# Kernel optimization log

Measured on AMD Instinct MI355X. Metric: run time of the kernel, lower is better.

Reference implementation:

```python
import jax, jax.numpy as jnp
import numpy as np


def setup_inputs() -> dict:
    key = jax.random.key(0)
    k1, k2, k3 = jax.random.split(key, 3)
    B, T, J, D = 32, 1024, 128, 256  # D = 2 * input_dim
    ctx_embd = jax.random.normal(k1, (B, T, D), dtype=jnp.float32)
    query_embd = jax.random.normal(k2, (B, J, D), dtype=jnp.float32)
    # nn.Linear(6*input_dim, 1, bias=False) weight flattened: [w1 | w2 | w3], each of size D
    w = jax.random.normal(k3, (3 * D,), dtype=jnp.float32) * (1.0 / np.sqrt(3 * D))
    return {"ctx_embd": ctx_embd, "query_embd": query_embd, "w": w}


def reference(ctx_embd, query_embd, w):
    D = ctx_embd.shape[-1]
    w1, w2, w3 = w[:D], w[D:2 * D], w[2 * D:]
    # Trilinear score S[b,t,j] = ctx.w1 + query.w2 + (ctx*query).w3, decomposed
    # (algebraically identical to Linear(cat(ctx, query, ctx*query))).
    s_ctx = ctx_embd @ w1            # [B, T]
    s_qry = query_embd @ w2          # [B, J]
    s_mul = jnp.einsum('btd,bjd->btj', ctx_embd * w3, query_embd)  # [B, T, J]
    S = s_ctx[:, :, None] + s_qry[:, None, :] + s_mul              # [B, T, J]
    # Context-to-query attention
    a = jax.nn.softmax(S, axis=-1)                                 # [B, T, J]
    c2q = jnp.einsum('btj,bjd->btd', a, query_embd)                # [B, T, D]
    # Query-to-context attention
    b = jax.nn.softmax(jnp.max(S, axis=2), axis=-1)                # [B, T]
    q2c = jnp.einsum('bt,btd->bd', b, ctx_embd)[:, None, :]        # [B, 1, D] broadcast over T
    G = jnp.concatenate(
        [ctx_embd, c2q, ctx_embd * c2q, ctx_embd * q2c], axis=-1)  # [B, T, 4D]
    return G
```

## Files before the change

kernel.cpp:

```cpp
#include <hip/hip_runtime.h>

typedef float f4 __attribute__((ext_vector_type(4)));
typedef short s8v __attribute__((ext_vector_type(8)));
typedef unsigned int u4v __attribute__((ext_vector_type(4)));

#define B_ 32
#define T_ 1024
#define J_ 128
#define D_ 256

__device__ inline unsigned short f2bf(float x) {
    unsigned int u = __float_as_uint(x);
    u += 0x7fffu + ((u >> 16) & 1u);
    return (unsigned short)(u >> 16);
}
__device__ inline float bf2f(unsigned short h) {
    return __uint_as_float(((unsigned int)h) << 16);
}

__global__ __launch_bounds__(256) void k_prep(const float* __restrict__ q, const float* __restrict__ w,
                                              unsigned short* __restrict__ Bqh, float* __restrict__ sq,
                                              float* __restrict__ q2c) {
    int bj = blockIdx.x;
    int d = threadIdx.x;
    if (bj < B_) q2c[bj * D_ + d] = 0.f;
    float qv = q[bj * D_ + d];
    float w1 = w[d], w2 = w[D_ + d], w3 = w[2 * D_ + d];
    Bqh[bj * D_ + d] = f2bf(w3 * qv + w1);
    float p = qv * w2;
#pragma unroll
    for (int m = 32; m >= 1; m >>= 1) p += __shfl_xor(p, m);
    __shared__ float red[4];
    if ((d & 63) == 0) red[d >> 6] = p;
    __syncthreads();
    if (d == 0) sq[bj] = red[0] + red[1] + red[2] + red[3];
}

__global__ __launch_bounds__(256) void k_tq(const float* __restrict__ q,
                                            unsigned short* __restrict__ qTh, unsigned short* __restrict__ qTl) {
    __shared__ float t_[64][65];
    int b = blockIdx.x >> 3, jt = (blockIdx.x >> 2) & 1, dt = blockIdx.x & 3;
    const float* qb = q + (b * J_ + jt * 64) * D_ + dt * 64;
#pragma unroll
    for (int i = 0; i < 16; i++) {
        int lin = threadIdx.x + 256 * i;
        int jj = lin >> 6, dd = lin & 63;
        t_[jj][dd] = qb[jj * D_ + dd];
    }
    __syncthreads();
#pragma unroll
    for (int i = 0; i < 16; i++) {
        int lin = threadIdx.x + 256 * i;
        int dd = lin >> 6, jj = lin & 63;
        float v = t_[jj][dd];
        unsigned short h = f2bf(v);
        unsigned short lo = f2bf(v - bf2f(h));
        int o = (b * D_ + dt * 64 + dd) * J_ + jt * 64 + jj;
        qTh[o] = h;
        qTl[o] = lo;
    }
}

__global__ __launch_bounds__(256, 3) void k_main(const float* __restrict__ ctx,
                                                 const unsigned short* __restrict__ Bqh,
                                                 const unsigned short* __restrict__ qTh,
                                                 const unsigned short* __restrict__ qTl,
                                                 const float* __restrict__ sq,
                                                 float* __restrict__ M, float* __restrict__ out) {
    __shared__ __align__(16) char lds[41472];
    char* Bs = lds;
    char* Ps = lds + 32768;
    float* sc = (float*)(lds + 40960);

    int b  = blockIdx.x >> 5;
    int t0 = (blockIdx.x & 31) << 5;
    int tid = threadIdx.x;
    int w = tid >> 6, l = tid & 63, lr = l & 15, lq = l >> 4;
    int rg = w & 1, ch = w >> 1;
    int R0 = rg << 4;

    const unsigned short* BqB  = Bqh + b * J_ * D_;
    const unsigned short* qThB = qTh + b * D_ * J_;
    const unsigned short* qTlB = qTl + b * D_ * J_;

    u4v h0[8], h1[8];
#pragma unroll
    for (int i = 0; i < 8; i++) {
        int g = tid + (i << 8);
        int jr = g >> 4, c = g & 15;
        h0[i] = *(const u4v*)(BqB + jr * D_ + c * 8);
    }
    const float* ctxA = ctx + (b * T_ + t0 + R0 + lr) * D_;
    s8v af[8];
#pragma unroll
    for (int k = 0; k < 4; k++) {
        f4 a0 = *(const f4*)(ctxA + k * 32 + lq * 8);
        f4 a1 = *(const f4*)(ctxA + k * 32 + lq * 8 + 4);
        union { unsigned short u[8]; s8v v; } t;
#pragma unroll
        for (int e = 0; e < 4; e++) { t.u[e] = f2bf(a0[e]); t.u[e + 4] = f2bf(a1[e]); }
        af[k] = t.v;
    }
#pragma unroll
    for (int i = 0; i < 8; i++) {
        int g = tid + (i << 8);
        int jr = g >> 4, c = g & 15;
        h1[i] = *(const u4v*)(BqB + jr * D_ + 128 + c * 8);
    }
#pragma unroll
    for (int k = 4; k < 8; k++) {
        f4 a0 = *(const f4*)(ctxA + k * 32 + lq * 8);
        f4 a1 = *(const f4*)(ctxA + k * 32 + lq * 8 + 4);
        union { unsigned short u[8]; s8v v; } t;
#pragma unroll
        for (int e = 0; e < 4; e++) { t.u[e] = f2bf(a0[e]); t.u[e + 4] = f2bf(a1[e]); }
        af[k] = t.v;
    }

#pragma unroll
    for (int i = 0; i < 8; i++) {
        int g = tid + (i << 8);
        int jr = g >> 4, c = g & 15;
        *(u4v*)(Bs + jr * 256 + ((c ^ (jr & 7)) << 4)) = h0[i];
    }

    f4 acc[4];
#pragma unroll
    for (int nf = 0; nf < 4; nf++) acc[nf] = (f4){0.f, 0.f, 0.f, 0.f};

    __syncthreads();
#pragma unroll
    for (int k2 = 0; k2 < 4; k2++)
#pragma unroll
        for (int nf = 0; nf < 4; nf++) {
            int jr = (ch << 6) + (nf << 4) + lr;
            s8v bv = *(const s8v*)(Bs + jr * 256 + ((((k2 << 2) + lq) ^ (jr & 7)) << 4));
            acc[nf] = __builtin_amdgcn_mfma_f32_16x16x32_bf16(af[k2], bv, acc[nf], 0, 0, 0);
        }
    __syncthreads();
#pragma unroll
    for (int i = 0; i < 8; i++) {
        int g = tid + (i << 8);
        int jr = g >> 4, c = g & 15;
        *(u4v*)(Bs + jr * 256 + ((c ^ (jr & 7)) << 4)) = h1[i];
    }
    u4v qreg[4];
#pragma unroll
    for (int i = 0; i < 4; i++) {
        int g = tid + (i << 8);
        int dr = g >> 4, c = g & 15;
        qreg[i] = *(const u4v*)(qThB + dr * J_ + c * 8);
    }
    __syncthreads();
#pragma unroll
    for (int k2 = 0; k2 < 4; k2++)
#pragma unroll
        for (int nf = 0; nf < 4; nf++) {
            int jr = (ch << 6) + (nf << 4) + lr;
            s8v bv = *(const s8v*)(Bs + jr * 256 + ((((k2 << 2) + lq) ^ (jr & 7)) << 4));
            acc[nf] = __builtin_amdgcn_mfma_f32_16x16x32_bf16(af[4 + k2], bv, acc[nf], 0, 0, 0);
        }

    float sqv[4];
#pragma unroll
    for (int nf = 0; nf < 4; nf++) sqv[nf] = sq[b * J_ + (ch << 6) + (nf << 4) + lr];
    float mp[4], sp[4];
#pragma unroll
    for (int r = 0; r < 4; r++) {
        float m = -1e30f;
#pragma unroll
        for (int nf = 0; nf < 4; nf++) { acc[nf][r] += sqv[nf]; m = fmaxf(m, acc[nf][r]); }
#pragma unroll
        for (int msk = 8; msk >= 1; msk >>= 1) m = fmaxf(m, __shfl_xor(m, msk));
        float s = 0.f;
#pragma unroll
        for (int nf = 0; nf < 4; nf++) { float e = __expf(acc[nf][r] - m); acc[nf][r] = e; s += e; }
#pragma unroll
        for (int msk = 8; msk >= 1; msk >>= 1) s += __shfl_xor(s, msk);
        mp[r] = m; sp[r] = s;
        if (lr == 0) {
            int row = R0 + (lq << 2) + r;
            sc[(row << 2) + (ch << 1)] = m;
            sc[(row << 2) + (ch << 1) + 1] = s;
        }
    }
    __syncthreads();

#pragma unroll
    for (int i = 0; i < 4; i++) {
        int g = tid + (i << 8);
        int dr = g >> 4, c = g & 15;
        *(u4v*)(Bs + dr * 256 + ((c ^ (dr & 7)) << 4)) = qreg[i];
    }
#pragma unroll
    for (int i = 0; i < 4; i++) {
        int g = tid + (i << 8);
        int dr = g >> 4, c = g & 15;
        qreg[i] = *(const u4v*)(qThB + (64 + dr) * J_ + c * 8);
    }

#pragma unroll
    for (int r = 0; r < 4; r++) {
        int row = R0 + (lq << 2) + r;
        float m0 = sc[(row << 2)],     s0 = sc[(row << 2) + 1];
        float m1 = sc[(row << 2) + 2], s1 = sc[(row << 2) + 3];
        float m = fmaxf(m0, m1);
        float sum = s0 * __expf(m0 - m) + s1 * __expf(m1 - m);
        float scale = __expf(mp[r] - m) / sum;
#pragma unroll
        for (int nf = 0; nf < 4; nf++) {
            int cc = (ch << 6) + (nf << 4) + lr;
            int chunk = cc >> 3;
            *(unsigned short*)(Ps + row * 256 + ((chunk ^ (row & 7)) << 4) + ((lr & 7) << 1)) =
                f2bf(acc[nf][r] * scale);
        }
        if (ch == 0 && lr == 0) M[b * T_ + t0 + row] = m;
    }
    __syncthreads();

    int dh2 = w >> 1;
    int prow = R0 + lr;
    s8v pf[4];
#pragma unroll
    for (int jk = 0; jk < 4; jk++)
        pf[jk] = *(const s8v*)(Ps + prow * 256 + ((((jk << 2) + lq) ^ (prow & 7)) << 4));

    f4 acc2[8];
#pragma unroll
    for (int ai = 0; ai < 8; ai++) acc2[ai] = (f4){0.f, 0.f, 0.f, 0.f};

#pragma unroll
    for (int s = 0; s < 8; s++) {
        char* rb = Bs + ((s & 1) << 14);
        if (s < 7) {
            char* wb = Bs + (((s + 1) & 1) << 14);
#pragma unroll
            for (int i = 0; i < 4; i++) {
                int g = tid + (i << 8);
                int dr = g >> 4, c = g & 15;
                *(u4v*)(wb + dr * 256 + ((c ^ (dr & 7)) << 4)) = qreg[i];
            }
        }
        if (s < 6) {
            const unsigned short* src = (s + 2 < 4) ? (qThB + ((s + 2) << 6) * J_)
                                                    : (qTlB + ((s - 2) << 6) * J_);
#pragma unroll
            for (int i = 0; i < 4; i++) {
                int g = tid + (i << 8);
                int dr = g >> 4, c = g & 15;
                qreg[i] = *(const u4v*)(src + dr * J_ + c * 8);
            }
        }
#pragma unroll
        for (int df2 = 0; df2 < 2; df2++) {
            int dr = (((dh2 << 1) + df2) << 4) + lr;
            int ai = ((s & 3) << 1) + df2;
#pragma unroll
            for (int jk = 0; jk < 4; jk++) {
                s8v bv = *(const s8v*)(rb + dr * 256 + ((((jk << 2) + lq) ^ (dr & 7)) << 4));
                acc2[ai] = __builtin_amdgcn_mfma_f32_16x16x32_bf16(pf[jk], bv, acc2[ai], 0, 0, 0);
            }
        }
        if (s < 7) __syncthreads();
    }
    __syncthreads();

    float* cq = (float*)Bs;
#pragma unroll
    for (int s2 = 0; s2 < 4; s2++)
#pragma unroll
        for (int df2 = 0; df2 < 2; df2++) {
            int col = (s2 << 6) + (dh2 << 5) + (df2 << 4) + lr;
            int ai = (s2 << 1) + df2;
            int chunk = col >> 2;
#pragma unroll
            for (int r = 0; r < 4; r++) {
                int row = R0 + (lq << 2) + r;
                *(float*)((char*)cq + (row << 10) + ((chunk ^ (row & 7)) << 4) + ((col & 3) << 2)) = acc2[ai][r];
            }
        }
    __syncthreads();

    int row = tid >> 3;
    int o = b * T_ + t0 + row;
    const float* crow = ctx + o * D_;
    float* orow = out + o * 1024;
#pragma unroll
    for (int i = 0; i < 8; i++) {
        int col4 = (i << 5) + ((tid & 7) << 2);
        int chunk = col4 >> 2;
        f4 val = *(const f4*)((char*)cq + (row << 10) + ((chunk ^ (row & 7)) << 4));
        f4 cx = *(const f4*)(crow + col4);
        *(f4*)(orow + col4) = cx;
        *(f4*)(orow + 256 + col4) = val;
        *(f4*)(orow + 512 + col4) = cx * val;
    }
}

__global__ __launch_bounds__(256) void k_q2c(const float* __restrict__ ctx, const float* __restrict__ M,
                                             float* __restrict__ q2c) {
    int b = blockIdx.x >> 5, tc = blockIdx.x & 31;
    int tid = threadIdx.x;
    const float* Mb = M + b * T_;

    float v0 = Mb[tid], v1 = Mb[tid + 256], v2 = Mb[tid + 512], v3 = Mb[tid + 768];
    float mx = fmaxf(fmaxf(v0, v1), fmaxf(v2, v3));
#pragma unroll
    for (int m = 32; m >= 1; m >>= 1) mx = fmaxf(mx, __shfl_xor(mx, m));
    __shared__ float rA[4], rB[4], wt[32];
    if ((tid & 63) == 0) rA[tid >> 6] = mx;
    __syncthreads();
    mx = fmaxf(fmaxf(rA[0], rA[1]), fmaxf(rA[2], rA[3]));

    float sm = __expf(v0 - mx) + __expf(v1 - mx) + __expf(v2 - mx) + __expf(v3 - mx);
#pragma unroll
    for (int m = 32; m >= 1; m >>= 1) sm += __shfl_xor(sm, m);
    if ((tid & 63) == 0) rB[tid >> 6] = sm;
    if (tid < 32) wt[tid] = __expf(Mb[tc * 32 + tid] - mx);
    __syncthreads();
    sm = rB[0] + rB[1] + rB[2] + rB[3];

    float acc = 0.f;
    const float* cb = ctx + (b * T_ + tc * 32) * D_ + tid;
#pragma unroll 8
    for (int tt = 0; tt < 32; tt++) acc += wt[tt] * cb[tt * D_];
    atomicAdd(&q2c[b * D_ + tid], acc / sm);
}

__global__ __launch_bounds__(256) void k_out4(const float* __restrict__ ctx, const float* __restrict__ q2c,
                                              float* __restrict__ out) {
    int idx = blockIdx.x * 256 + threadIdx.x;
    int e = idx * 4;
    int b = e >> 18;
    int t = (e >> 8) & 1023;
    int d = e & 255;
    f4 cv = *(const f4*)&ctx[e];
    f4 qv = *(const f4*)&q2c[b * D_ + d];
    *(f4*)&out[(b * T_ + t) * 1024 + 768 + d] = cv * qv;
}

extern "C" void kernel_launch(void* const* d_in, const int* in_sizes, int n_in,
                              void* d_out, int out_size, void* d_ws, size_t ws_size,
                              hipStream_t stream) {
    const float* ctx   = (const float*)d_in[0];
    const float* query = (const float*)d_in[1];
    const float* w     = (const float*)d_in[2];
    float* out = (float*)d_out;

    unsigned short* Bqh = (unsigned short*)d_ws;
    unsigned short* qTh = Bqh + B_ * J_ * D_;
    unsigned short* qTl = qTh + B_ * J_ * D_;
    float* fws = (float*)(qTl + B_ * J_ * D_);
    float* sq  = fws;
    float* M   = fws + 4096;
    float* q2c = fws + 4096 + 32768;

    k_prep<<<B_ * J_, 256, 0, stream>>>(query, w, Bqh, sq, q2c);
    k_tq<<<B_ * 2 * 4, 256, 0, stream>>>(query, qTh, qTl);
    k_main<<<B_ * (T_ / 32), 256, 0, stream>>>(ctx, Bqh, qTh, qTl, sq, M, out);
    k_q2c<<<B_ * 32, 256, 0, stream>>>(ctx, M, q2c);
    k_out4<<<(B_ * T_ * D_ / 4) / 256, 256, 0, stream>>>(ctx, q2c, out);
}
```

Before: 69.71 us.

## Use global_load_lds double-buffered staging, drop bf16 low-part query split, nontemporal stores

Replaces register-staged global-to-LDS copies of the query operands with direct global_load_lds async loads into two ping-pong LDS buffers, pipelining staging with the MFMA phases. It removes the hi/lo bf16 split of the transposed query (qTl), halving the c2q GEMM work and the loads for it at the cost of c2q precision. Output stores become nontemporal to avoid polluting cache. The reduced precision may risk tolerance failures.

```diff
diff --git a/kernel.cpp b/kernel.cpp
--- a/kernel.cpp
+++ b/kernel.cpp
@@ -2,7 +2,6 @@
 
 typedef float f4 __attribute__((ext_vector_type(4)));
 typedef short s8v __attribute__((ext_vector_type(8)));
-typedef unsigned int u4v __attribute__((ext_vector_type(4)));
 
 #define B_ 32
 #define T_ 1024
@@ -14,8 +13,11 @@
     u += 0x7fffu + ((u >> 16) & 1u);
     return (unsigned short)(u >> 16);
 }
-__device__ inline float bf2f(unsigned short h) {
-    return __uint_as_float(((unsigned int)h) << 16);
+
+__device__ __forceinline__ void ldsload16(const void* g, void* l) {
+    __builtin_amdgcn_global_load_lds(
+        (const __attribute__((address_space(1))) void*)g,
+        (__attribute__((address_space(3))) void*)l, 16, 0, 0);
 }
 
 __global__ __launch_bounds__(256) void k_prep(const float* __restrict__ q, const float* __restrict__ w,
@@ -37,7 +39,7 @@
 }
 
 __global__ __launch_bounds__(256) void k_tq(const float* __restrict__ q,
-                                            unsigned short* __restrict__ qTh, unsigned short* __restrict__ qTl) {
+                                            unsigned short* __restrict__ qTh) {
     __shared__ float t_[64][65];
     int b = blockIdx.x >> 3, jt = (blockIdx.x >> 2) & 1, dt = blockIdx.x & 3;
     const float* qb = q + (b * J_ + jt * 64) * D_ + dt * 64;
@@ -52,23 +54,18 @@
     for (int i = 0; i < 16; i++) {
         int lin = threadIdx.x + 256 * i;
         int dd = lin >> 6, jj = lin & 63;
-        float v = t_[jj][dd];
-        unsigned short h = f2bf(v);
-        unsigned short lo = f2bf(v - bf2f(h));
-        int o = (b * D_ + dt * 64 + dd) * J_ + jt * 64 + jj;
-        qTh[o] = h;
-        qTl[o] = lo;
+        qTh[(b * D_ + dt * 64 + dd) * J_ + jt * 64 + jj] = f2bf(t_[jj][dd]);
     }
 }
 
 __global__ __launch_bounds__(256, 3) void k_main(const float* __restrict__ ctx,
                                                  const unsigned short* __restrict__ Bqh,
                                                  const unsigned short* __restrict__ qTh,
-                                                 const unsigned short* __restrict__ qTl,
                                                  const float* __restrict__ sq,
                                                  float* __restrict__ M, float* __restrict__ out) {
     __shared__ __align__(16) char lds[41472];
-    char* Bs = lds;
+    char* B0 = lds;
+    char* B1 = lds + 16384;
     char* Ps = lds + 32768;
     float* sc = (float*)(lds + 40960);
 
@@ -81,90 +78,78 @@
 
     const unsigned short* BqB  = Bqh + b * J_ * D_;
     const unsigned short* qThB = qTh + b * D_ * J_;
-    const unsigned short* qTlB = qTl + b * D_ * J_;
-
-    u4v h0[8], h1[8];
-#pragma unroll
-    for (int i = 0; i < 8; i++) {
-        int g = tid + (i << 8);
-        int jr = g >> 4, c = g & 15;
-        h0[i] = *(const u4v*)(BqB + jr * D_ + c * 8);
-    }
+
+    auto stageBq = [&](char* buf, int qt) {
+#pragma unroll
+        for (int i = 0; i < 4; i++) {
+            int g = tid + (i << 8);
+            int jr = g >> 3, c = g & 7;
+            ldsload16(BqB + jr * D_ + (qt << 6) + ((c ^ (jr & 7)) << 3),
+                      buf + (i << 12) + (w << 10));
+        }
+    };
+    auto stageQ = [&](char* buf, int st) {
+#pragma unroll
+        for (int i = 0; i < 4; i++) {
+            int g = tid + (i << 8);
+            int dr = g >> 4, c = g & 15;
+            ldsload16(qThB + ((st << 6) + dr) * J_ + ((c ^ (dr & 7)) << 3),
+                      buf + (i << 12) + (w << 10));
+        }
+    };
+
+    f4 acc[4];
+#pragma unroll
+    for (int nf = 0; nf < 4; nf++) acc[nf] = (f4){0.f, 0.f, 0.f, 0.f};
+
+    stageBq(B0, 0);
+    stageBq(B1, 1);
+
     const float* ctxA = ctx + (b * T_ + t0 + R0 + lr) * D_;
     s8v af[8];
-#pragma unroll
-    for (int k = 0; k < 4; k++) {
-        f4 a0 = *(const f4*)(ctxA + k * 32 + lq * 8);
-        f4 a1 = *(const f4*)(ctxA + k * 32 + lq * 8 + 4);
-        union { unsigned short u[8]; s8v v; } t;
-#pragma unroll
-        for (int e = 0; e < 4; e++) { t.u[e] = f2bf(a0[e]); t.u[e + 4] = f2bf(a1[e]); }
-        af[k] = t.v;
-    }
-#pragma unroll
-    for (int i = 0; i < 8; i++) {
-        int g = tid + (i << 8);
-        int jr = g >> 4, c = g & 15;
-        h1[i] = *(const u4v*)(BqB + jr * D_ + 128 + c * 8);
-    }
-#pragma unroll
-    for (int k = 4; k < 8; k++) {
-        f4 a0 = *(const f4*)(ctxA + k * 32 + lq * 8);
-        f4 a1 = *(const f4*)(ctxA + k * 32 + lq * 8 + 4);
-        union { unsigned short u[8]; s8v v; } t;
-#pragma unroll
-        for (int e = 0; e < 4; e++) { t.u[e] = f2bf(a0[e]); t.u[e + 4] = f2bf(a1[e]); }
-        af[k] = t.v;
-    }
-
-#pragma unroll
-    for (int i = 0; i < 8; i++) {
-        int g = tid + (i << 8);
-        int jr = g >> 4, c = g & 15;
-        *(u4v*)(Bs + jr * 256 + ((c ^ (jr & 7)) << 4)) = h0[i];
-    }
-
-    f4 acc[4];
-#pragma unroll
-    for (int nf = 0; nf < 4; nf++) acc[nf] = (f4){0.f, 0.f, 0.f, 0.f};
-
-    __syncthreads();
-#pragma unroll
-    for (int k2 = 0; k2 < 4; k2++)
-#pragma unroll
-        for (int nf = 0; nf < 4; nf++) {
-            int jr = (ch << 6) + (nf << 4) + lr;
-            s8v bv = *(const s8v*)(Bs + jr * 256 + ((((k2 << 2) + lq) ^ (jr & 7)) << 4));
-            acc[nf] = __builtin_amdgcn_mfma_f32_16x16x32_bf16(af[k2], bv, acc[nf], 0, 0, 0);
-        }
-    __syncthreads();
-#pragma unroll
-    for (int i = 0; i < 8; i++) {
-        int g = tid + (i << 8);
-        int jr = g >> 4, c = g & 15;
-        *(u4v*)(Bs + jr * 256 + ((c ^ (jr & 7)) << 4)) = h1[i];
-    }
-    u4v qreg[4];
-#pragma unroll
-    for (int i = 0; i < 4; i++) {
-        int g = tid + (i << 8);
-        int dr = g >> 4, c = g & 15;
-        qreg[i] = *(const u4v*)(qThB + dr * J_ + c * 8);
-    }
-    __syncthreads();
-#pragma unroll
-    for (int k2 = 0; k2 < 4; k2++)
-#pragma unroll
-        for (int nf = 0; nf < 4; nf++) {
-            int jr = (ch << 6) + (nf << 4) + lr;
-            s8v bv = *(const s8v*)(Bs + jr * 256 + ((((k2 << 2) + lq) ^ (jr & 7)) << 4));
-            acc[nf] = __builtin_amdgcn_mfma_f32_16x16x32_bf16(af[4 + k2], bv, acc[nf], 0, 0, 0);
-        }
+    {
+        f4 c0[8], c1[8];
+#pragma unroll
+        for (int k = 0; k < 8; k++) {
+            c0[k] = *(const f4*)(ctxA + k * 32 + lq * 8);
+            c1[k] = *(const f4*)(ctxA + k * 32 + lq * 8 + 4);
+        }
+#pragma unroll
+        for (int k = 0; k < 8; k++) {
+            union { unsigned short u[8]; s8v v; } t;
+#pragma unroll
+            for (int e = 0; e < 4; e++) { t.u[e] = f2bf(c0[k][e]); t.u[e + 4] = f2bf(c1[k][e]); }
+            af[k] = t.v;
+        }
+    }
+
+    auto mfmaA = [&](char* buf, int qt) {
+#pragma unroll
+        for (int kk = 0; kk < 2; kk++)
+#pragma unroll
+            for (int nf = 0; nf < 4; nf++) {
+                int jr = (ch << 6) + (nf << 4) + lr;
+                s8v bv = *(const s8v*)(buf + (jr << 7) + ((((kk << 2) | lq) ^ (jr & 7)) << 4));
+                acc[nf] = __builtin_amdgcn_mfma_f32_16x16x32_bf16(af[(qt << 1) | kk], bv, acc[nf], 0, 0, 0);
+            }
+    };
+
+    __syncthreads();
+    mfmaA(B0, 0);
+    __syncthreads();
+    stageBq(B0, 2);
+    mfmaA(B1, 1);
+    __syncthreads();
+    stageBq(B1, 3);
+    mfmaA(B0, 2);
+    __syncthreads();
+    stageQ(B0, 0);
+    mfmaA(B1, 3);
 
     float sqv[4];
 #pragma unroll
     for (int nf = 0; nf < 4; nf++) sqv[nf] = sq[b * J_ + (ch << 6) + (nf << 4) + lr];
-    float mp[4], sp[4];
+    float mp[4];
 #pragma unroll
     for (int r = 0; r < 4; r++) {
         float m = -1e30f;
@@ -177,7 +162,7 @@
         for (int nf = 0; nf < 4; nf++) { float e = __expf(acc[nf][r] - m); acc[nf][r] = e; s += e; }
 #pragma unroll
         for (int msk = 8; msk >= 1; msk >>= 1) s += __shfl_xor(s, msk);
-        mp[r] = m; sp[r] = s;
+        mp[r] = m;
         if (lr == 0) {
             int row = R0 + (lq << 2) + r;
             sc[(row << 2) + (ch << 1)] = m;
@@ -185,19 +170,7 @@
         }
     }
     __syncthreads();
-
-#pragma unroll
-    for (int i = 0; i < 4; i++) {
-        int g = tid + (i << 8);
-        int dr = g >> 4, c = g & 15;
-        *(u4v*)(Bs + dr * 256 + ((c ^ (dr & 7)) << 4)) = qreg[i];
-    }
-#pragma unroll
-    for (int i = 0; i < 4; i++) {
-        int g = tid + (i << 8);
-        int dr = g >> 4, c = g & 15;
-        qreg[i] = *(const u4v*)(qThB + (64 + dr) * J_ + c * 8);
-    }
+    stageQ(B1, 1);
 
 #pragma unroll
     for (int r = 0; r < 4; r++) {
@@ -229,43 +202,31 @@
 #pragma unroll
     for (int ai = 0; ai < 8; ai++) acc2[ai] = (f4){0.f, 0.f, 0.f, 0.f};
 
-#pragma unroll
-    for (int s = 0; s < 8; s++) {
-        char* rb = Bs + ((s & 1) << 14);
-        if (s < 7) {
-            char* wb = Bs + (((s + 1) & 1) << 14);
-#pragma unroll
-            for (int i = 0; i < 4; i++) {
-                int g = tid + (i << 8);
-                int dr = g >> 4, c = g & 15;
-                *(u4v*)(wb + dr * 256 + ((c ^ (dr & 7)) << 4)) = qreg[i];
-            }
-        }
-        if (s < 6) {
-            const unsigned short* src = (s + 2 < 4) ? (qThB + ((s + 2) << 6) * J_)
-                                                    : (qTlB + ((s - 2) << 6) * J_);
-#pragma unroll
-            for (int i = 0; i < 4; i++) {
-                int g = tid + (i << 8);
-                int dr = g >> 4, c = g & 15;
-                qreg[i] = *(const u4v*)(src + dr * J_ + c * 8);
-            }
-        }
+    auto mfmaB = [&](char* rb, int s) {
 #pragma unroll
         for (int df2 = 0; df2 < 2; df2++) {
-            int dr = (((dh2 << 1) + df2) << 4) + lr;
-            int ai = ((s & 3) << 1) + df2;
+            int dr = (dh2 << 5) + (df2 << 4) + lr;
+            int ai = (s << 1) + df2;
 #pragma unroll
             for (int jk = 0; jk < 4; jk++) {
-                s8v bv = *(const s8v*)(rb + dr * 256 + ((((jk << 2) + lq) ^ (dr & 7)) << 4));
+                s8v bv = *(const s8v*)(rb + (dr << 8) + ((((jk << 2) + lq) ^ (dr & 7)) << 4));
                 acc2[ai] = __builtin_amdgcn_mfma_f32_16x16x32_bf16(pf[jk], bv, acc2[ai], 0, 0, 0);
             }
         }
-        if (s < 7) __syncthreads();
-    }
-    __syncthreads();
-
-    float* cq = (float*)Bs;
+    };
+
+    mfmaB(B0, 0);
+    __syncthreads();
+    stageQ(B0, 2);
+    mfmaB(B1, 1);
+    __syncthreads();
+    stageQ(B1, 3);
+    mfmaB(B0, 2);
+    __syncthreads();
+    mfmaB(B1, 3);
+    __syncthreads();
+
+    float* cq = (float*)lds;
 #pragma unroll
     for (int s2 = 0; s2 < 4; s2++)
 #pragma unroll
@@ -291,9 +252,10 @@
         int chunk = col4 >> 2;
         f4 val = *(const f4*)((char*)cq + (row << 10) + ((chunk ^ (row & 7)) << 4));
         f4 cx = *(const f4*)(crow + col4);
-        *(f4*)(orow + col4) = cx;
-        *(f4*)(orow + 256 + col4) = val;
-        *(f4*)(orow + 512 + col4) = cx * val;
+        f4 v3 = cx * val;
+        __builtin_nontemporal_store(cx, (f4*)(orow + col4));
+        __builtin_nontemporal_store(val, (f4*)(orow + 256 + col4));
+        __builtin_nontemporal_store(v3, (f4*)(orow + 512 + col4));
     }
 }
 
@@ -336,7 +298,8 @@
     int d = e & 255;
     f4 cv = *(const f4*)&ctx[e];
     f4 qv = *(const f4*)&q2c[b * D_ + d];
-    *(f4*)&out[(b * T_ + t) * 1024 + 768 + d] = cv * qv;
+    f4 r = cv * qv;
+    __builtin_nontemporal_store(r, (f4*)&out[(b * T_ + t) * 1024 + 768 + d]);
 }
 
 extern "C" void kernel_launch(void* const* d_in, const int* in_sizes, int n_in,
@@ -349,15 +312,14 @@
 
     unsigned short* Bqh = (unsigned short*)d_ws;
     unsigned short* qTh = Bqh + B_ * J_ * D_;
-    unsigned short* qTl = qTh + B_ * J_ * D_;
-    float* fws = (float*)(qTl + B_ * J_ * D_);
+    float* fws = (float*)(qTh + B_ * J_ * D_);
     float* sq  = fws;
     float* M   = fws + 4096;
     float* q2c = fws + 4096 + 32768;
 
     k_prep<<<B_ * J_, 256, 0, stream>>>(query, w, Bqh, sq, q2c);
-    k_tq<<<B_ * 2 * 4, 256, 0, stream>>>(query, qTh, qTl);
-    k_main<<<B_ * (T_ / 32), 256, 0, stream>>>(ctx, Bqh, qTh, qTl, sq, M, out);
+    k_tq<<<B_ * 2 * 4, 256, 0, stream>>>(query, qTh);
+    k_main<<<B_ * (T_ / 32), 256, 0, stream>>>(ctx, Bqh, qTh, sq, M, out);
     k_q2c<<<B_ * 32, 256, 0, stream>>>(ctx, M, q2c);
     k_out4<<<(B_ * T_ * D_ / 4) / 256, 256, 0, stream>>>(ctx, q2c, out);
 }
```

Result: faster. 67.29 us (-3.5%).
